# Optimization experiments

Measured on AMD Instinct MI355X. Metric: run time of the kernel, lower is better.

Reference implementation:

```python
import jax, jax.numpy as jnp
import numpy as np

N = 4096     # batch of positions
E = 32       # descriptor buckets (experts)
NBLK = 12    # residual blocks per head


def _ln(x, g, b, eps=1e-5):
    m = x.mean(-1, keepdims=True)
    v = ((x - m) ** 2).mean(-1, keepdims=True)
    return (x - m) / jnp.sqrt(v + eps) * g + b


def _gelu(x):
    return jax.nn.gelu(x, approximate=False)  # torch nn.GELU default = exact erf


def setup_inputs() -> dict:
    key = jax.random.key(0)
    ks = iter(jax.random.split(key, 64))

    def nrm(shape, scale=0.05):
        return jax.random.normal(next(ks), shape, jnp.float32) * scale

    return {
        "piece_idx": jax.random.randint(next(ks), (N, 64), 0, 12),
        "side_flag": jax.random.randint(next(ks), (N,), 0, 2),
        "ep_file": jax.random.randint(next(ks), (N,), 0, 8),
        "castle_ms": jax.random.uniform(next(ks), (N, 4), jnp.float32),
        "fifty_a": jax.random.uniform(next(ks), (N,), jnp.float32),
        "descriptor_index": jax.random.randint(next(ks), (N,), 0, E),
        # per-bucket embedding tables, stacked on a leading expert axis
        "Wp_w": nrm((E, 64, 12, 32)), "Wp_b": nrm((E, 64, 12, 32)),
        "Wc_w": nrm((E, 4, 32)), "Wc_b": nrm((E, 4, 32)),
        "Wep_w": nrm((E, 8, 32)), "Wep_b": nrm((E, 8, 32)),
        "Wf_w": nrm((E, 2, 32)), "Wf_b": nrm((E, 2, 32)),
        # per-bucket MLP head params (weights stored as [in,out])
        "fc1_w": nrm((E, 2240, 256)), "fc1_b": nrm((E, 256)),
        "ln1_g": jnp.ones((E, 256)), "ln1_b": jnp.zeros((E, 256)),
        "fc2_w": nrm((E, 256, 32)), "fc2_b": nrm((E, 32)),
        "ln2_g": jnp.ones((E, 32)), "ln2_b": jnp.zeros((E, 32)),
        "blkA_w": nrm((NBLK, E, 32, 32)), "blkA_b": nrm((NBLK, E, 32)),
        "blkA_g": jnp.ones((NBLK, E, 32)), "blkA_be": jnp.zeros((NBLK, E, 32)),
        "blkB_w": nrm((NBLK, E, 32, 32)), "blkB_b": nrm((NBLK, E, 32)),
        "blkB_g": jnp.ones((NBLK, E, 32)), "blkB_be": jnp.zeros((NBLK, E, 32)),
        "out_w": nrm((E, 32, 51)), "out_b": nrm((E, 51)),
        "bins": jnp.linspace(0.0, 1.0, 51),
    }


def reference(piece_idx, side_flag, ep_file, castle_ms, fifty_a, descriptor_index,
              Wp_w, Wp_b, Wc_w, Wc_b, Wep_w, Wep_b, Wf_w, Wf_b,
              fc1_w, fc1_b, ln1_g, ln1_b, fc2_w, fc2_b, ln2_g, ln2_b,
              blkA_w, blkA_b, blkA_g, blkA_be, blkB_w, blkB_b, blkB_g, blkB_be,
              out_w, out_b, bins):
    desc = descriptor_index
    side = side_flag.astype(bool)
    n = piece_idx.shape[0]

    # ---- per-bucket, side-selected embedding gathers -> x_emb [N,2240] ----
    sq = jnp.arange(64)
    pc = jnp.maximum(piece_idx, 0)                                 # clamp -1 -> 0
    w_emb = Wp_w[desc[:, None], sq[None, :], pc]                    # [N,64,32]
    b_emb = Wp_b[desc[:, None], sq[None, :], pc]
    piece_emb = jnp.where(side[:, None, None], b_emb, w_emb)
    piece_emb = piece_emb * (piece_idx >= 0)[..., None].astype(piece_emb.dtype)
    pieces_vec = piece_emb.reshape(n, 2048)

    Wc = jnp.where(side[:, None, None], Wc_b[desc], Wc_w[desc])     # [N,4,32]
    castle_vec = (castle_ms[..., None] * Wc).reshape(n, 128)

    Wep = jnp.where(side[:, None, None], Wep_b[desc], Wep_w[desc])  # [N,8,32]
    epc = jnp.maximum(ep_file, 0)
    ep_vec = jnp.take_along_axis(Wep, epc[:, None, None], axis=1)[:, 0]
    ep_vec = ep_vec * (ep_file >= 0)[:, None].astype(ep_vec.dtype)

    Wf = jnp.where(side[:, None, None], Wf_b[desc], Wf_w[desc])     # [N,2,32]
    fifty_vec = (1.0 - fifty_a)[:, None] * Wf[:, 0] + fifty_a[:, None] * Wf[:, 1]

    x = jnp.concatenate([pieces_vec, castle_vec, ep_vec, fifty_vec], axis=1)  # [N,2240]

    # ---- expert-routed dense layer: all-expert GEMM + per-token select ----
    def dense_moe(h, W, b):
        ha = jnp.einsum('nd,edh->neh', h, W)                        # [N,E,out]
        hsel = jnp.take_along_axis(ha, desc[:, None, None], axis=1)[:, 0]
        return hsel + b[desc]

    h = _ln(_gelu(dense_moe(x, fc1_w, fc1_b)), ln1_g[desc], ln1_b[desc])   # [N,256]
    h = _ln(_gelu(dense_moe(h, fc2_w, fc2_b)), ln2_g[desc], ln2_b[desc])   # [N,32]

    def blk(carry, p):
        wA, bA, gA, beA, wB, bB, gB, beB = p
        y = _ln(_gelu(dense_moe(carry, wA, bA)), gA[desc], beA[desc])
        y = _ln(_gelu(dense_moe(y, wB, bB)), gB[desc], beB[desc])
        return carry + y, None

    h, _ = jax.lax.scan(blk, h, (blkA_w, blkA_b, blkA_g, blkA_be,
                                 blkB_w, blkB_b, blkB_g, blkB_be))

    logits = dense_moe(_gelu(h), out_w, out_b)                      # [N,51]
    p_win = jnp.sum(jax.nn.softmax(logits, axis=-1) * bins, axis=-1, keepdims=True)
    return logits, p_win
```

## Files before the change

kernel.cpp:

```cpp
#include <hip/hip_runtime.h>
#include <math.h>

#define N 4096
#define E 32
#define NBLK 12
#define D_IN 2240
#define H1 256
#define H2 32
#define NOUT 51
#define MT 16
#define NPAD (N + E*(MT-1))
#define NTILE (NPAD/MT)
#define KSPLIT 4
#define NROWS 4608
#define GMAX 96

typedef short s8v __attribute__((ext_vector_type(8)));
typedef float f4v __attribute__((ext_vector_type(4)));

__device__ __forceinline__ float gelu(float x){
    return 0.5f * x * (1.0f + erff(x * 0.70710678118654752f));
}
__device__ __forceinline__ unsigned short f2bf(float f){
    unsigned int u = __float_as_uint(f);
    unsigned int r = (u + 0x7fffu + ((u >> 16) & 1u)) >> 16;
    return (unsigned short)r;
}
__device__ __forceinline__ float bflo(unsigned int u){ return __uint_as_float(u << 16); }
__device__ __forceinline__ float bfhi(unsigned int u){ return __uint_as_float(u & 0xffff0000u); }

template<int CTRL>
__device__ __forceinline__ float dppadd(float x){
    int y = __builtin_amdgcn_update_dpp(0, __float_as_int(x), CTRL, 0xF, 0xF, true);
    return x + __int_as_float(y);
}
__device__ __forceinline__ float red32(float x){
    x = dppadd<0x121>(x);
    x = dppadd<0x122>(x);
    x = dppadd<0x124>(x);
    x = dppadd<0x128>(x);
    int y = __builtin_amdgcn_ds_swizzle(__float_as_int(x), 0x401F);
    return x + __int_as_float(y);
}

__global__ void k_prep(const int* __restrict__ piece_idx,
                       const int* __restrict__ side_flag,
                       const int* __restrict__ ep_file,
                       const float* __restrict__ castle_ms,
                       const float* __restrict__ fifty_a,
                       const int* __restrict__ desc_idx,
                       const float* __restrict__ Wp_w, const float* __restrict__ Wp_b,
                       const float* __restrict__ Wc_w, const float* __restrict__ Wc_b,
                       const float* __restrict__ Wep_w, const float* __restrict__ Wep_b,
                       const float* __restrict__ Wf_w, const float* __restrict__ Wf_b,
                       unsigned short* __restrict__ xs,
                       int* __restrict__ perm, int* __restrict__ tile_e,
                       int4* __restrict__ garr, int* __restrict__ ngroups){
    int tid = threadIdx.x;
    if (blockIdx.x == 0){
        __shared__ int scnt[E];
        __shared__ int spoff[E+1];
        __shared__ int scur[E];
        if (tid < E) scnt[tid] = 0;
        __syncthreads();
        for (int n = tid; n < N; n += blockDim.x) atomicAdd(&scnt[desc_idx[n]], 1);
        __syncthreads();
        if (tid == 0){
            int run = 0;
            for (int e = 0; e < E; e++){ spoff[e] = run; run += ((scnt[e] + MT - 1)/MT)*MT; }
            spoff[E] = run;
            int ng = 0;
            for (int e = 0; e < E; e++){
                int t0 = spoff[e]/MT, t1 = spoff[e+1]/MT;
                for (int t = t0; t < t1; t += 8){
                    int nv = t1 - t; if (nv > 8) nv = 8;
                    if (ng < GMAX) garr[ng] = make_int4(t, e, nv, 0);
                    ng++;
                }
            }
            *ngroups = (ng > GMAX) ? GMAX : ng;
        }
        __syncthreads();
        if (tid < E) scur[tid] = spoff[tid];
        for (int p = tid; p < NPAD + 64; p += blockDim.x) perm[p] = -1;
        __syncthreads();
        for (int n = tid; n < N; n += blockDim.x){
            int p = atomicAdd(&scur[desc_idx[n]], 1);
            perm[p] = n;
        }
        for (int t = tid; t < NTILE; t += blockDim.x){
            int p0 = t*MT;
            int e = -1;
            if (p0 < spoff[E]){
                for (int q = 0; q < E; q++){
                    if (p0 >= spoff[q] && p0 < spoff[q+1]){ e = q; break; }
                }
            }
            tile_e[t] = e;
        }
        s8v z = {0,0,0,0,0,0,0,0};
        for (int i = tid; i < D_IN/8; i += blockDim.x)
            *(s8v*)(xs + (size_t)N*D_IN + i*8) = z;
        return;
    }
    int row = blockIdx.x - 1;
    unsigned short* xr = xs + (size_t)row * D_IN;
    int d = desc_idx[row];
    int s = side_flag[row];
    __shared__ int pidx[64];
    if (tid < 64) pidx[tid] = piece_idx[row*64 + tid];
    __syncthreads();
    const float* Wp  = s ? Wp_b  : Wp_w;
    const float* Wc  = s ? Wc_b  : Wc_w;
    const float* Wep = s ? Wep_b : Wep_w;
    const float* Wf  = s ? Wf_b  : Wf_w;
    int ep  = ep_file[row];
    int epc = ep > 0 ? ep : 0;
    float a = fifty_a[row];
    for (int t = tid; t < D_IN/8; t += blockDim.x){
        int i0 = t*8;
        float v[8];
        if (i0 < 2048){
            int sq = i0 >> 5, c0 = i0 & 31;
            int pc = pidx[sq];
            float msk = pc >= 0 ? 1.0f : 0.0f;
            int pcc = pc > 0 ? pc : 0;
            const float* base = Wp + (((size_t)d*64 + sq)*12 + pcc)*32 + c0;
            float4 a0 = *(const float4*)base;
            float4 a1 = *(const float4*)(base + 4);
            v[0]=a0.x*msk; v[1]=a0.y*msk; v[2]=a0.z*msk; v[3]=a0.w*msk;
            v[4]=a1.x*msk; v[5]=a1.y*msk; v[6]=a1.z*msk; v[7]=a1.w*msk;
        } else if (i0 < 2176){
            int j = i0 - 2048; int ci = j >> 5, c0 = j & 31;
            float cv = castle_ms[row*4 + ci];
            const float* base = Wc + ((size_t)d*4 + ci)*32 + c0;
            float4 a0 = *(const float4*)base;
            float4 a1 = *(const float4*)(base + 4);
            v[0]=a0.x*cv; v[1]=a0.y*cv; v[2]=a0.z*cv; v[3]=a0.w*cv;
            v[4]=a1.x*cv; v[5]=a1.y*cv; v[6]=a1.z*cv; v[7]=a1.w*cv;
        } else if (i0 < 2208){
            int c0 = i0 - 2176;
            float msk = ep >= 0 ? 1.0f : 0.0f;
            const float* base = Wep + ((size_t)d*8 + epc)*32 + c0;
            float4 a0 = *(const float4*)base;
            float4 a1 = *(const float4*)(base + 4);
            v[0]=a0.x*msk; v[1]=a0.y*msk; v[2]=a0.z*msk; v[3]=a0.w*msk;
            v[4]=a1.x*msk; v[5]=a1.y*msk; v[6]=a1.z*msk; v[7]=a1.w*msk;
        } else {
            int c0 = i0 - 2208;
            #pragma unroll
            for (int j = 0; j < 8; j++)
                v[j] = (1.0f - a) * Wf[(size_t)d*64 + c0 + j] + a * Wf[(size_t)d*64 + 32 + c0 + j];
        }
        s8v p;
        #pragma unroll
        for (int j = 0; j < 8; j++) p[j] = (short)f2bf(v[j]);
        *(s8v*)(xr + i0) = p;
    }
}

__launch_bounds__(256)
__global__ void k_fc1(const int4* __restrict__ garr, const int* __restrict__ ngroups,
                      const unsigned short* __restrict__ xs,
                      const int* __restrict__ perm,
                      const float* __restrict__ W1,
                      float* __restrict__ h1p){
    int g = blockIdx.x;
    if (g >= *ngroups) return;
    int4 gi = garr[g];
    int tile0 = gi.x, e = gi.y, nv = gi.z;
    int kc = blockIdx.y, nh = blockIdx.z;
    int kstart = (kc <= 2) ? kc*18 : 53;
    int nsteps = (kc < 2) ? 18 : 17;
    int tid = threadIdx.x;
    int lane = tid & 63, wave = tid >> 6;
    int quad = lane >> 4, l16 = lane & 15;

    __shared__ float bst[32][133];

    const unsigned short* Arow[8];
    #pragma unroll
    for (int mt = 0; mt < 8; mt++){
        int p = perm[(tile0 + mt)*MT + l16];
        if (p < 0) p = N;
        Arow[mt] = xs + (size_t)p*D_IN + quad*8;
    }

    const float* Wb = W1 + (size_t)e*D_IN*H1 + nh*128;
    int kk0 = tid >> 5;
    int nq4 = (tid & 31) << 2;
    int cl0 = wave*32 + l16;
    int cl1 = cl0 + 16;

    f4v acc[8][2];
    #pragma unroll
    for (int mt = 0; mt < 8; mt++){ acc[mt][0] = (f4v){0.f,0.f,0.f,0.f}; acc[mt][1] = (f4v){0.f,0.f,0.f,0.f}; }

    int kend = kstart + nsteps;
    for (int s = kstart; s < kend; s++){
        int kb = s*32;
        #pragma unroll
        for (int p = 0; p < 4; p++){
            int kk = p*8 + kk0;
            float4 v = *(const float4*)(Wb + (size_t)(kb + kk)*H1 + nq4);
            bst[kk][nq4]   = v.x;
            bst[kk][nq4+1] = v.y;
            bst[kk][nq4+2] = v.z;
            bst[kk][nq4+3] = v.w;
        }
        __syncthreads();
        s8v b0, b1;
        #pragma unroll
        for (int j = 0; j < 8; j++){
            b0[j] = (short)f2bf(bst[quad*8 + j][cl0]);
            b1[j] = (short)f2bf(bst[quad*8 + j][cl1]);
        }
        #pragma unroll
        for (int mt = 0; mt < 8; mt++){
            s8v av = *(const s8v*)(Arow[mt] + kb);
            acc[mt][0] = __builtin_amdgcn_mfma_f32_16x16x32_bf16(av, b0, acc[mt][0], 0, 0, 0);
            acc[mt][1] = __builtin_amdgcn_mfma_f32_16x16x32_bf16(av, b1, acc[mt][1], 0, 0, 0);
        }
        __syncthreads();
    }
    int col0 = nh*128 + wave*32 + l16;
    float* out = h1p + (size_t)kc*NROWS*H1;
    #pragma unroll
    for (int mt = 0; mt < 8; mt++){
        if (mt >= nv) break;
        int posb = (tile0 + mt)*MT + quad*4;
        #pragma unroll
        for (int r = 0; r < 4; r++){
            out[(size_t)(posb + r)*H1 + col0]      = acc[mt][0][r];
            out[(size_t)(posb + r)*H1 + col0 + 16] = acc[mt][1][r];
        }
    }
}

__launch_bounds__(256)
__global__ void k_tail(const int* __restrict__ tile_e, const int* __restrict__ perm,
                       const float* __restrict__ h1p, const float* __restrict__ b1,
                       const float* __restrict__ g1, const float* __restrict__ be1,
                       const float* __restrict__ W2, const float* __restrict__ b2,
                       const float* __restrict__ g2, const float* __restrict__ be2,
                       const float* __restrict__ Aw, const float* __restrict__ Abv,
                       const float* __restrict__ Ag, const float* __restrict__ Abe,
                       const float* __restrict__ Bw, const float* __restrict__ Bb,
                       const float* __restrict__ Bg, const float* __restrict__ Bbe,
                       const float* __restrict__ Ow, const float* __restrict__ Ob,
                       const float* __restrict__ bins,
                       float* __restrict__ out){
    int th = blockIdx.x;
    int t  = th >> 1;
    int r0 = (th & 1) * 8;
    int e = tile_e[t];
    if (e < 0) return;
    int tid = threadIdx.x;

    __shared__ __align__(16) float        shf[8*260];
    __shared__ __align__(16) unsigned int W2pk[4096];
    __shared__ __align__(16) float        vecs[NBLK*6*32];
    __shared__ __align__(16) unsigned int wbuf[2][1024];
    __shared__ __align__(16) float        sh2[8][36];
    __shared__ __align__(16) float        sh3[8][36];

    {
        const float* W2e = W2 + (size_t)e*H1*H2;
        for (int j = tid; j < 4096; j += 256){
            int h = j & 1, q = j >> 1, cc = q & 31, p2 = q >> 5;
            int k0 = 4*p2 + 2*h;
            unsigned int lo = f2bf(W2e[k0*32 + cc]);
            unsigned int hi = f2bf(W2e[(k0+1)*32 + cc]);
            W2pk[(p2*32 + cc)*2 + h] = lo | (hi << 16);
        }
    }
    for (int j = tid; j < NBLK*6*32; j += 256){
        int cc = j & 31, vi = (j >> 5) % 6, tb = j / 192;
        size_t wb = (size_t)tb*E + e;
        const float* src;
        switch(vi){ case 0: src=Abv; break; case 1: src=Ag; break; case 2: src=Abe; break;
                    case 3: src=Bb;  break; case 4: src=Bg; break; default: src=Bbe; }
        vecs[j] = src[wb*32 + cc];
    }
    {
        size_t base = (size_t)e*1024;
        #pragma unroll
        for (int k = 0; k < 4; k++){
            int s_all = k*256 + tid;
            int s = s_all & 511;
            int h = s & 1, q = s >> 1, cc = q & 31, p2 = q >> 5;
            int k0 = 4*p2 + 2*h;
            const float* src = (s_all >> 9) ? Bw : Aw;
            unsigned int lo = f2bf(src[base + k0*32 + cc]);
            unsigned int hi = f2bf(src[base + (k0+1)*32 + cc]);
            wbuf[0][s_all] = lo | (hi << 16);
        }
    }
    #pragma unroll
    for (int it = 0; it < 2; it++){
        int slot = it*256 + tid;
        int r = slot >> 6, c4 = (slot & 63) << 2;
        int row = t*MT + r0 + r;
        float4 v = {0.f,0.f,0.f,0.f};
        #pragma unroll
        for (int kc = 0; kc < KSPLIT; kc++){
            float4 p = *(const float4*)(h1p + ((size_t)kc*NROWS + row)*H1 + c4);
            v.x += p.x; v.y += p.y; v.z += p.z; v.w += p.w;
        }
        float4 bb = *(const float4*)(b1 + e*H1 + c4);
        shf[r*260 + c4]   = gelu(v.x + bb.x);
        shf[r*260 + c4+1] = gelu(v.y + bb.y);
        shf[r*260 + c4+2] = gelu(v.z + bb.z);
        shf[r*260 + c4+3] = gelu(v.w + bb.w);
    }
    __syncthreads();

    int m = tid >> 5, c = tid & 31;
    {
        float s = 0.f, s2 = 0.f;
        #pragma unroll
        for (int j = 0; j < 8; j++){
            float x = shf[m*260 + c + 32*j];
            s += x; s2 += x*x;
        }
        s  = red32(s);
        s2 = red32(s2);
        float mean = s * (1.0f/H1);
        float var  = s2 * (1.0f/H1) - mean*mean;
        float rs = rsqrtf(var + 1e-5f);
        #pragma unroll
        for (int j = 0; j < 8; j++){
            int k = c + 32*j;
            shf[m*260 + k] = (shf[m*260 + k] - mean) * rs * g1[e*H1 + k] + be1[e*H1 + k];
        }
    }
    float hv;
    {
        const uint2* W2p = (const uint2*)W2pk;
        float q0=0.f,q1=0.f,q2=0.f,q3=0.f;
        #pragma unroll 8
        for (int p2 = 0; p2 < 64; p2++){
            uint2 w = W2p[p2*32 + c];
            float4 h4 = *(const float4*)(shf + m*260 + p2*4);
            q0 = fmaf(h4.x, bflo(w.x), q0);
            q1 = fmaf(h4.y, bfhi(w.x), q1);
            q2 = fmaf(h4.z, bflo(w.y), q2);
            q3 = fmaf(h4.w, bfhi(w.y), q3);
        }
        float acc = (q0+q1) + (q2+q3) + b2[e*H2 + c];
        float y = gelu(acc);
        float s  = red32(y);
        float s2 = red32(y*y);
        float mean2 = s * (1.0f/H2);
        float var2  = s2 * (1.0f/H2) - mean2*mean2;
        hv = (y - mean2) * rsqrtf(var2 + 1e-5f) * g2[e*H2+c] + be2[e*H2+c];
    }

    int cur = 0;
    for (int tb = 0; tb < NBLK; tb++){
        float wfa[4], wfb[4];
        int tbn = tb + 1;
        if (tbn < NBLK){
            size_t base = ((size_t)tbn*E + e)*1024;
            #pragma unroll
            for (int k = 0; k < 4; k++){
                int s_all = k*256 + tid;
                int s = s_all & 511;
                int h = s & 1, q = s >> 1, cc = q & 31, p2 = q >> 5;
                int k0 = 4*p2 + 2*h;
                const float* src = (s_all >> 9) ? Bw : Aw;
                wfa[k] = src[base + k0*32 + cc];
                wfb[k] = src[base + (k0+1)*32 + cc];
            }
        }
        const float* vA = &vecs[tb*192];
        const uint2* WA = (const uint2*)&wbuf[cur][0];
        const uint2* WB = (const uint2*)&wbuf[cur][512];
        sh2[m][c] = hv;
        float q0=0.f,q1=0.f,q2=0.f,q3=0.f;
        #pragma unroll
        for (int p2 = 0; p2 < 8; p2++){
            uint2 w = WA[p2*32 + c];
            float4 h4 = *(const float4*)(&sh2[m][p2*4]);
            q0 = fmaf(h4.x, bflo(w.x), q0);
            q1 = fmaf(h4.y, bfhi(w.x), q1);
            q2 = fmaf(h4.z, bflo(w.y), q2);
            q3 = fmaf(h4.w, bfhi(w.y), q3);
        }
        float ya = (q0+q1) + (q2+q3) + vA[c];
        ya = gelu(ya);
        float sa  = red32(ya);
        float sa2 = red32(ya*ya);
        float ma = sa * (1.0f/H2);
        float va = sa2 * (1.0f/H2) - ma*ma;
        float yA = (ya - ma) * rsqrtf(va + 1e-5f) * vA[32+c] + vA[64+c];
        sh3[m][c] = yA;
        q0=0.f; q1=0.f; q2=0.f; q3=0.f;
        #pragma unroll
        for (int p2 = 0; p2 < 8; p2++){
            uint2 w = WB[p2*32 + c];
            float4 h4 = *(const float4*)(&sh3[m][p2*4]);
            q0 = fmaf(h4.x, bflo(w.x), q0);
            q1 = fmaf(h4.y, bfhi(w.x), q1);
            q2 = fmaf(h4.z, bflo(w.y), q2);
            q3 = fmaf(h4.w, bfhi(w.y), q3);
        }
        float yb = (q0+q1) + (q2+q3) + vA[96+c];
        yb = gelu(yb);
        float sb  = red32(yb);
        float sb2 = red32(yb*yb);
        float mb = sb * (1.0f/H2);
        float vb = sb2 * (1.0f/H2) - mb*mb;
        hv += (yb - mb) * rsqrtf(vb + 1e-5f) * vA[128+c] + vA[160+c];
        if (tbn < NBLK){
            #pragma unroll
            for (int k = 0; k < 4; k++){
                int s_all = k*256 + tid;
                unsigned int lo = f2bf(wfa[k]);
                unsigned int hi = f2bf(wfb[k]);
                wbuf[cur^1][s_all] = lo | (hi << 16);
            }
        }
        cur ^= 1;
        __syncthreads();
    }

    sh2[m][c] = gelu(hv);
    __syncthreads();
    int wave = tid >> 6, lane = tid & 63;
    const float* W = Ow + (size_t)e*32*NOUT;
    for (int rr = wave; rr < 8; rr += 4){
        int orow = perm[t*MT + r0 + rr];
        if (orow < 0) continue;
        float acc = (lane < NOUT) ? Ob[e*NOUT + lane] : -INFINITY;
        #pragma unroll
        for (int k = 0; k < 32; k++){
            float gk = sh2[rr][k];
            if (lane < NOUT) acc = fmaf(gk, W[k*NOUT + lane], acc);
        }
        if (lane < NOUT) out[(size_t)orow*NOUT + lane] = acc;
        float mx = acc;
        #pragma unroll
        for (int o = 32; o > 0; o >>= 1) mx = fmaxf(mx, __shfl_xor(mx, o));
        float pp = (lane < NOUT) ? expf(acc - mx) : 0.0f;
        float sum = pp;
        float pb = (lane < NOUT) ? pp * bins[lane] : 0.0f;
        float sb = pb;
        #pragma unroll
        for (int o = 32; o > 0; o >>= 1){ sum += __shfl_xor(sum, o); sb += __shfl_xor(sb, o); }
        if (lane == 0) out[(size_t)N*NOUT + orow] = sb / sum;
    }
}

extern "C" void kernel_launch(void* const* d_in, const int* in_sizes, int n_in,
                              void* d_out, int out_size, void* d_ws, size_t ws_size,
                              hipStream_t stream){
    const int*   piece_idx = (const int*)d_in[0];
    const int*   side_flag = (const int*)d_in[1];
    const int*   ep_file   = (const int*)d_in[2];
    const float* castle_ms = (const float*)d_in[3];
    const float* fifty_a   = (const float*)d_in[4];
    const int*   desc      = (const int*)d_in[5];
    const float* Wp_w  = (const float*)d_in[6];
    const float* Wp_b  = (const float*)d_in[7];
    const float* Wc_w  = (const float*)d_in[8];
    const float* Wc_b  = (const float*)d_in[9];
    const float* Wep_w = (const float*)d_in[10];
    const float* Wep_b = (const float*)d_in[11];
    const float* Wf_w  = (const float*)d_in[12];
    const float* Wf_b  = (const float*)d_in[13];
    const float* fc1_w = (const float*)d_in[14];
    const float* fc1_b = (const float*)d_in[15];
    const float* ln1_g = (const float*)d_in[16];
    const float* ln1_b = (const float*)d_in[17];
    const float* fc2_w = (const float*)d_in[18];
    const float* fc2_b = (const float*)d_in[19];
    const float* ln2_g = (const float*)d_in[20];
    const float* ln2_b = (const float*)d_in[21];
    const float* blkA_w  = (const float*)d_in[22];
    const float* blkA_b  = (const float*)d_in[23];
    const float* blkA_g  = (const float*)d_in[24];
    const float* blkA_be = (const float*)d_in[25];
    const float* blkB_w  = (const float*)d_in[26];
    const float* blkB_b  = (const float*)d_in[27];
    const float* blkB_g  = (const float*)d_in[28];
    const float* blkB_be = (const float*)d_in[29];
    const float* out_w = (const float*)d_in[30];
    const float* out_b = (const float*)d_in[31];
    const float* bins  = (const float*)d_in[32];

    char* wsp = (char*)d_ws;
    auto alloc = [&](size_t bytes){ void* p = (void*)wsp; wsp += (bytes + 255) & ~(size_t)255; return p; };
    int*            perm    = (int*)            alloc((size_t)(NPAD+128)*4);
    int*            tile_e  = (int*)            alloc((size_t)NTILE*4);
    int4*           garr    = (int4*)           alloc((size_t)GMAX*16);
    int*            ngroups = (int*)            alloc(256);
    unsigned short* xs      = (unsigned short*) alloc((size_t)(N+128)*D_IN*2);
    float*          h1p     = (float*)          alloc((size_t)KSPLIT*NROWS*H1*4);

    k_prep<<<1 + N, 256, 0, stream>>>(piece_idx, side_flag, ep_file,
                                      castle_ms, fifty_a, desc,
                                      Wp_w, Wp_b, Wc_w, Wc_b,
                                      Wep_w, Wep_b, Wf_w, Wf_b,
                                      xs, perm, tile_e, garr, ngroups);
    k_fc1<<<dim3(GMAX, KSPLIT, 2), 256, 0, stream>>>(garr, ngroups, xs, perm, fc1_w, h1p);
    k_tail<<<NTILE*2, 256, 0, stream>>>(tile_e, perm, h1p, fc1_b, ln1_g, ln1_b,
                                        fc2_w, fc2_b, ln2_g, ln2_b,
                                        blkA_w, blkA_b, blkA_g, blkA_be,
                                        blkB_w, blkB_b, blkB_g, blkB_be,
                                        out_w, out_b, bins, (float*)d_out);
}
```

Measured before the change: 282.6 us.

## Prepack bf16 tail weights in a separate kernel and read residual weights from global

Adds a k_pack kernel that converts fc2 and the residual block weights to packed bf16 once per call into workspace buffers. k_tail then copies the prepacked fc2 tile into LDS directly and reads the residual block weights straight from global (L2-cached) instead of converting them per block. This drops the double-buffered LDS staging and the per-iteration __syncthreads. The cost is an extra kernel launch plus global-latency reads inside the 12-block residual loop.

After: 280.9 us. Within noise of the previous version (-0.6%).

```diff
diff --git a/kernel.cpp b/kernel.cpp
--- a/kernel.cpp
+++ b/kernel.cpp
@@ -41,6 +41,34 @@
     x = dppadd<0x128>(x);
     int y = __builtin_amdgcn_ds_swizzle(__float_as_int(x), 0x401F);
     return x + __int_as_float(y);
+}
+
+__global__ void k_pack(const float* __restrict__ W2,
+                       const float* __restrict__ Aw, const float* __restrict__ Bw,
+                       unsigned int* __restrict__ w2pk_g, unsigned int* __restrict__ rpk_g){
+    int j = blockIdx.x*256 + threadIdx.x;
+    if (j < E*4096){
+        int e = j >> 12, idx = j & 4095;
+        int h = idx & 1, q = idx >> 1, cc = q & 31, p2 = q >> 5;
+        int k0 = 4*p2 + 2*h;
+        const float* W2e = W2 + (size_t)e*H1*H2;
+        unsigned int lo = f2bf(W2e[k0*32 + cc]);
+        unsigned int hi = f2bf(W2e[(k0+1)*32 + cc]);
+        w2pk_g[((size_t)e << 12) + (p2*32 + cc)*2 + h] = lo | (hi << 16);
+    } else {
+        int i = j - E*4096;
+        int slot = i & 511;
+        int m = i >> 9;
+        int e = m & 31, mat = m >> 5;
+        int tb = mat >> 1, s = mat & 1;
+        int h = slot & 1, q = slot >> 1, cc = q & 31, p2 = q >> 5;
+        int k0 = 4*p2 + 2*h;
+        const float* src = s ? Bw : Aw;
+        size_t base = ((size_t)tb*E + e)*1024;
+        unsigned int lo = f2bf(src[base + k0*32 + cc]);
+        unsigned int hi = f2bf(src[base + (k0+1)*32 + cc]);
+        rpk_g[((size_t)m << 9) + slot] = lo | (hi << 16);
+    }
 }
 
 __global__ void k_prep(const int* __restrict__ piece_idx,
@@ -241,12 +269,13 @@
 __global__ void k_tail(const int* __restrict__ tile_e, const int* __restrict__ perm,
                        const float* __restrict__ h1p, const float* __restrict__ b1,
                        const float* __restrict__ g1, const float* __restrict__ be1,
-                       const float* __restrict__ W2, const float* __restrict__ b2,
+                       const unsigned int* __restrict__ w2pk_g, const float* __restrict__ b2,
                        const float* __restrict__ g2, const float* __restrict__ be2,
-                       const float* __restrict__ Aw, const float* __restrict__ Abv,
-                       const float* __restrict__ Ag, const float* __restrict__ Abe,
-                       const float* __restrict__ Bw, const float* __restrict__ Bb,
-                       const float* __restrict__ Bg, const float* __restrict__ Bbe,
+                       const unsigned int* __restrict__ rpk,
+                       const float* __restrict__ Abv, const float* __restrict__ Ag,
+                       const float* __restrict__ Abe,
+                       const float* __restrict__ Bb, const float* __restrict__ Bg,
+                       const float* __restrict__ Bbe,
                        const float* __restrict__ Ow, const float* __restrict__ Ob,
                        const float* __restrict__ bins,
                        float* __restrict__ out){
@@ -260,19 +289,12 @@
     __shared__ __align__(16) float        shf[8*260];
     __shared__ __align__(16) unsigned int W2pk[4096];
     __shared__ __align__(16) float        vecs[NBLK*6*32];
-    __shared__ __align__(16) unsigned int wbuf[2][1024];
     __shared__ __align__(16) float        sh2[8][36];
     __shared__ __align__(16) float        sh3[8][36];
 
     {
-        const float* W2e = W2 + (size_t)e*H1*H2;
-        for (int j = tid; j < 4096; j += 256){
-            int h = j & 1, q = j >> 1, cc = q & 31, p2 = q >> 5;
-            int k0 = 4*p2 + 2*h;
-            unsigned int lo = f2bf(W2e[k0*32 + cc]);
-            unsigned int hi = f2bf(W2e[(k0+1)*32 + cc]);
-            W2pk[(p2*32 + cc)*2 + h] = lo | (hi << 16);
-        }
+        const unsigned int* src = w2pk_g + ((size_t)e << 12);
+        for (int j = tid; j < 4096; j += 256) W2pk[j] = src[j];
     }
     for (int j = tid; j < NBLK*6*32; j += 256){
         int cc = j & 31, vi = (j >> 5) % 6, tb = j / 192;
@@ -281,20 +303,6 @@
         switch(vi){ case 0: src=Abv; break; case 1: src=Ag; break; case 2: src=Abe; break;
                     case 3: src=Bb;  break; case 4: src=Bg; break; default: src=Bbe; }
         vecs[j] = src[wb*32 + cc];
-    }
-    {
-        size_t base = (size_t)e*1024;
-        #pragma unroll
-        for (int k = 0; k < 4; k++){
-            int s_all = k*256 + tid;
-            int s = s_all & 511;
-            int h = s & 1, q = s >> 1, cc = q & 31, p2 = q >> 5;
-            int k0 = 4*p2 + 2*h;
-            const float* src = (s_all >> 9) ? Bw : Aw;
-            unsigned int lo = f2bf(src[base + k0*32 + cc]);
-            unsigned int hi = f2bf(src[base + (k0+1)*32 + cc]);
-            wbuf[0][s_all] = lo | (hi << 16);
-        }
     }
     #pragma unroll
     for (int it = 0; it < 2; it++){
@@ -356,26 +364,10 @@
         hv = (y - mean2) * rsqrtf(var2 + 1e-5f) * g2[e*H2+c] + be2[e*H2+c];
     }
 
-    int cur = 0;
     for (int tb = 0; tb < NBLK; tb++){
-        float wfa[4], wfb[4];
-        int tbn = tb + 1;
-        if (tbn < NBLK){
-            size_t base = ((size_t)tbn*E + e)*1024;
-            #pragma unroll
-            for (int k = 0; k < 4; k++){
-                int s_all = k*256 + tid;
-                int s = s_all & 511;
-                int h = s & 1, q = s >> 1, cc = q & 31, p2 = q >> 5;
-                int k0 = 4*p2 + 2*h;
-                const float* src = (s_all >> 9) ? Bw : Aw;
-                wfa[k] = src[base + k0*32 + cc];
-                wfb[k] = src[base + (k0+1)*32 + cc];
-            }
-        }
         const float* vA = &vecs[tb*192];
-        const uint2* WA = (const uint2*)&wbuf[cur][0];
-        const uint2* WB = (const uint2*)&wbuf[cur][512];
+        const uint2* WA = (const uint2*)(rpk + (((size_t)(tb*2+0)*E + e) << 9));
+        const uint2* WB = (const uint2*)(rpk + (((size_t)(tb*2+1)*E + e) << 9));
         sh2[m][c] = hv;
         float q0=0.f,q1=0.f,q2=0.f,q3=0.f;
         #pragma unroll
@@ -412,17 +404,6 @@
         float mb = sb * (1.0f/H2);
         float vb = sb2 * (1.0f/H2) - mb*mb;
         hv += (yb - mb) * rsqrtf(vb + 1e-5f) * vA[128+c] + vA[160+c];
-        if (tbn < NBLK){
-            #pragma unroll
-            for (int k = 0; k < 4; k++){
-                int s_all = k*256 + tid;
-                unsigned int lo = f2bf(wfa[k]);
-                unsigned int hi = f2bf(wfb[k]);
-                wbuf[cur^1][s_all] = lo | (hi << 16);
-            }
-        }
-        cur ^= 1;
-        __syncthreads();
     }
 
     sh2[m][c] = gelu(hv);
@@ -495,9 +476,12 @@
     int*            tile_e  = (int*)            alloc((size_t)NTILE*4);
     int4*           garr    = (int4*)           alloc((size_t)GMAX*16);
     int*            ngroups = (int*)            alloc(256);
+    unsigned int*   w2pk_g  = (unsigned int*)   alloc((size_t)E*4096*4);
+    unsigned int*   rpk     = (unsigned int*)   alloc((size_t)24*E*512*4);
     unsigned short* xs      = (unsigned short*) alloc((size_t)(N+128)*D_IN*2);
     float*          h1p     = (float*)          alloc((size_t)KSPLIT*NROWS*H1*4);
 
+    k_pack<<<2048, 256, 0, stream>>>(fc2_w, blkA_w, blkB_w, w2pk_g, rpk);
     k_prep<<<1 + N, 256, 0, stream>>>(piece_idx, side_flag, ep_file,
                                       castle_ms, fifty_a, desc,
                                       Wp_w, Wp_b, Wc_w, Wc_b,
@@ -505,8 +489,9 @@
                                       xs, perm, tile_e, garr, ngroups);
     k_fc1<<<dim3(GMAX, KSPLIT, 2), 256, 0, stream>>>(garr, ngroups, xs, perm, fc1_w, h1p);
     k_tail<<<NTILE*2, 256, 0, stream>>>(tile_e, perm, h1p, fc1_b, ln1_g, ln1_b,
-                                        fc2_w, fc2_b, ln2_g, ln2_b,
-                                        blkA_w, blkA_b, blkA_g, blkA_be,
-                                        blkB_w, blkB_b, blkB_g, blkB_be,
+                                        w2pk_g, fc2_b, ln2_g, ln2_b,
+                                        rpk,
+                                        blkA_b, blkA_g, blkA_be,
+                                        blkB_b, blkB_g, blkB_be,
                                         out_w, out_b, bins, (float*)d_out);
 }
```
